# Kernel optimization log

Hardware: AMD Instinct MI355X
Metric: run time of the kernel (lower is better)

The kernel has to match this reference:

```python
import jax, jax.numpy as jnp
import numpy as np

H_OUT, W_OUT = 48, 320


def setup_inputs() -> dict:
    key = jax.random.key(0)
    k1, k2, k3 = jax.random.split(key, 3)
    x = jax.random.normal(k1, (8, 64, 200, 320), dtype=jnp.float32)
    bboxes = jax.random.randint(k2, (256, 4), 0, 320, dtype=jnp.int32)
    box_img = jax.random.randint(k3, (256,), 0, 8, dtype=jnp.int32)
    return {"x": x, "bboxes": bboxes, "box_img": box_img}


def reference(x, bboxes, box_img):
    # x: [B, C, H, W]; bboxes: [N, 4] int (x0, y0, x1, y1); box_img: [N] image index
    B, C, H, W = x.shape
    x0 = jnp.clip(bboxes[:, 0], 0, W - 1)
    y0 = jnp.clip(bboxes[:, 1], 0, H - 1)
    x1 = jnp.clip(bboxes[:, 2], 0, W - 1)
    y1 = jnp.clip(bboxes[:, 3], 0, H - 1)
    x1 = jnp.maximum(x1, x0)
    y1 = jnp.maximum(y1, y0)
    # inclusive crop: height/width of each crop
    h = y1 - y0 + 1  # [N]
    w = x1 - x0 + 1  # [N]
    # F.interpolate default mode='nearest': src = floor(dst * in/out)
    i = jnp.arange(H_OUT, dtype=jnp.int32)
    j = jnp.arange(W_OUT, dtype=jnp.int32)
    rows = y0[:, None] + (i[None, :] * h[:, None]) // H_OUT  # [N, H_OUT]
    cols = x0[:, None] + (j[None, :] * w[:, None]) // W_OUT  # [N, W_OUT]
    # single fused gather: advanced indices broadcast to [N, H_OUT, W_OUT],
    # with the ':' channel slice moved to the last axis -> [N, H_OUT, W_OUT, C]
    g = x[box_img[:, None, None], :, rows[:, :, None], cols[:, None, :]]
    return jnp.transpose(g, (0, 3, 1, 2))  # [N, C, H_OUT, W_OUT]
```

## Files before the change

kernel.cpp:

```cpp
#include <hip/hip_runtime.h>

#define B_IN   8
#define C_CH   64
#define H_IN   200
#define W_IN   320
#define H_OUT  48
#define W_OUT  320
#define N_BOX  256

__global__ __launch_bounds__(W_OUT) void roi_crop_kernel(
    const float* __restrict__ x,
    const int*   __restrict__ bboxes,
    const int*   __restrict__ box_img,
    float*       __restrict__ out)
{
    const int i   = blockIdx.x;
    const int box = blockIdx.y;
    const int j   = threadIdx.x;

    int x0 = bboxes[box * 4 + 0];
    int y0 = bboxes[box * 4 + 1];
    int x1 = bboxes[box * 4 + 2];
    int y1 = bboxes[box * 4 + 3];

    x0 = min(max(x0, 0), W_IN - 1);
    y0 = min(max(y0, 0), H_IN - 1);
    x1 = min(max(x1, 0), W_IN - 1);
    y1 = min(max(y1, 0), H_IN - 1);
    x1 = max(x1, x0);
    y1 = max(y1, y0);

    const int h = y1 - y0 + 1;
    const int w = x1 - x0 + 1;

    const int r   = y0 + (i * h) / H_OUT;
    const int col = x0 + (j * w) / W_OUT;
    const int img = box_img[box];

    const float* __restrict__ src =
        x + (size_t)img * (C_CH * H_IN * W_IN) + (size_t)r * W_IN + col;
    float* __restrict__ dst =
        out + (size_t)box * (C_CH * H_OUT * W_OUT) + (size_t)i * W_OUT + j;

    #pragma unroll 8
    for (int c = 0; c < C_CH; ++c) {
        dst[(size_t)c * (H_OUT * W_OUT)] = src[(size_t)c * (H_IN * W_IN)];
    }
}

extern "C" void kernel_launch(void* const* d_in, const int* in_sizes, int n_in,
                              void* d_out, int out_size, void* d_ws, size_t ws_size,
                              hipStream_t stream) {
    const float* x       = (const float*)d_in[0];
    const int*   bboxes  = (const int*)d_in[1];
    const int*   box_img = (const int*)d_in[2];
    float*       out     = (float*)d_out;

    dim3 grid(H_OUT, N_BOX);
    dim3 block(W_OUT);
    roi_crop_kernel<<<grid, block, 0, stream>>>(x, bboxes, box_img, out);
}
```

Measured before the change: 1.073 ms.

## Stage full source rows in LDS per channel plane with vectorized loads

The grid changes from one block per (output row, box) looping over channels to one block per (channel, box). Each block loads the 48 selected full input rows with 16-byte vector loads into a 60 KB shared tile, then gathers columns from LDS and writes output rows with nontemporal stores. This replaces strided scalar gathers from global memory with coalesced vector reads. The cost is that entire rows are read even when the crop is narrow, and the large LDS footprint limits occupancy.

```diff
diff --git a/kernel.cpp b/kernel.cpp
--- a/kernel.cpp
+++ b/kernel.cpp
@@ -1,6 +1,5 @@
 #include <hip/hip_runtime.h>
 
-#define B_IN   8
 #define C_CH   64
 #define H_IN   200
 #define W_IN   320
@@ -8,15 +7,19 @@
 #define W_OUT  320
 #define N_BOX  256
 
-__global__ __launch_bounds__(W_OUT) void roi_crop_kernel(
+typedef float float4v __attribute__((ext_vector_type(4), aligned(16)));
+
+__global__ __launch_bounds__(320, 2) void roi_crop_kernel(
     const float* __restrict__ x,
     const int*   __restrict__ bboxes,
     const int*   __restrict__ box_img,
     float*       __restrict__ out)
 {
-    const int i   = blockIdx.x;
+    __shared__ float tile[H_OUT * W_OUT];
+
+    const int c   = blockIdx.x;
     const int box = blockIdx.y;
-    const int j   = threadIdx.x;
+    const int t   = threadIdx.x;
 
     int x0 = bboxes[box * 4 + 0];
     int y0 = bboxes[box * 4 + 1];
@@ -32,19 +35,34 @@
 
     const int h = y1 - y0 + 1;
     const int w = x1 - x0 + 1;
-
-    const int r   = y0 + (i * h) / H_OUT;
-    const int col = x0 + (j * w) / W_OUT;
     const int img = box_img[box];
 
-    const float* __restrict__ src =
-        x + (size_t)img * (C_CH * H_IN * W_IN) + (size_t)r * W_IN + col;
-    float* __restrict__ dst =
-        out + (size_t)box * (C_CH * H_OUT * W_OUT) + (size_t)i * W_OUT + j;
+    const float* __restrict__ plane_in =
+        x + ((size_t)img * C_CH + c) * (H_IN * W_IN);
+    float* __restrict__ plane_out =
+        out + ((size_t)box * C_CH + c) * (H_OUT * W_OUT);
 
+    float4v v[12];
+    #pragma unroll
+    for (int k = 0; k < 12; ++k) {
+        const int p   = t + k * 320;
+        const int i   = p / 80;
+        const int wrd = p % 80;
+        const int r   = y0 + (i * h) / H_OUT;
+        v[k] = *(const float4v*)(plane_in + (size_t)r * W_IN + wrd * 4);
+    }
+    #pragma unroll
+    for (int k = 0; k < 12; ++k) {
+        const int p = t + k * 320;
+        *(float4v*)&tile[p * 4] = v[k];
+    }
+    __syncthreads();
+
+    const int col = x0 + (t * w) / W_OUT;
     #pragma unroll 8
-    for (int c = 0; c < C_CH; ++c) {
-        dst[(size_t)c * (H_OUT * W_OUT)] = src[(size_t)c * (H_IN * W_IN)];
+    for (int i = 0; i < H_OUT; ++i) {
+        const float val = tile[i * W_OUT + col];
+        __builtin_nontemporal_store(val, plane_out + i * W_OUT + t);
     }
 }
 
@@ -56,7 +74,7 @@
     const int*   box_img = (const int*)d_in[2];
     float*       out     = (float*)d_out;
 
-    dim3 grid(H_OUT, N_BOX);
-    dim3 block(W_OUT);
+    dim3 grid(C_CH, N_BOX);
+    dim3 block(320);
     roi_crop_kernel<<<grid, block, 0, stream>>>(x, bboxes, box_img, out);
 }
```

New measurement: 1.053 ms. No clear change (-1.9%).
